# Performance work log

Hardware: AMD Instinct MI355X
Metric: run time of the kernel (lower is better)

## Reference

```python
import jax, jax.numpy as jnp
import numpy as np

B, L = 4, 2048
D_MODEL, D_INNER, D_STATE, DT_RANK, K = 512, 1024, 16, 64, 4


def setup_inputs() -> dict:
    key = jax.random.key(0)
    ks = jax.random.split(key, 21)
    def n(k, shape, s=0.02):
        return (jax.random.normal(k, shape) * s).astype(jnp.float32)
    inp = {"x": jax.random.normal(ks[0], (B, L, D_MODEL), jnp.float32)}
    for i, sfx in enumerate(("f", "b")):
        o = 1 + i * 8
        inp[f"W_in_{sfx}"] = n(ks[o], (2 * D_INNER, D_MODEL))
        inp[f"conv_w_{sfx}"] = n(ks[o + 1], (D_INNER, 1, K), 0.1)
        inp[f"conv_b_{sfx}"] = jnp.zeros((D_INNER,), jnp.float32)
        inp[f"A_log_{sfx}"] = (jax.random.normal(ks[o + 2], (D_STATE, D_INNER)) * 0.1).astype(jnp.float32)
        inp[f"D_{sfx}"] = jnp.ones((D_INNER,), jnp.float32)
        inp[f"Wx_{sfx}"] = n(ks[o + 3], (DT_RANK + 2 * D_STATE, D_INNER))
        inp[f"Wdt_{sfx}"] = n(ks[o + 4], (D_INNER, DT_RANK), DT_RANK ** -0.5)
        dt = jnp.exp(jax.random.uniform(ks[o + 5], (D_INNER,)) * (np.log(0.1) - np.log(0.001)) + np.log(0.001))
        inp[f"bdt_{sfx}"] = (dt + jnp.log(-jnp.expm1(-dt))).astype(jnp.float32)
        inp[f"Wout_{sfx}"] = n(ks[o + 6], (D_MODEL, D_INNER))
    return inp


def _mamba_block(x, W_in, conv_w, conv_b, A_log, Dp, Wx, Wdt, bdt, Wout):
    # x: [B, L, d_model]
    xz = jnp.einsum('bld,ed->ble', x, W_in)              # [B, L, 2*d_inner]
    xb, zb = xz[..., :D_INNER], xz[..., D_INNER:]
    # causal depthwise conv over time
    xc = jnp.transpose(xb, (0, 2, 1))                     # [B, M, L]
    xc = jax.lax.conv_general_dilated(
        xc, conv_w, window_strides=(1,), padding=[(K - 1, 0)],
        feature_group_count=D_INNER,
        dimension_numbers=('NCH', 'OIH', 'NCH')) + conv_b[None, :, None]
    xb = jax.nn.silu(jnp.transpose(xc, (0, 2, 1)))        # [B, L, M]
    # input-dependent SSM parameters
    proj = jnp.einsum('blm,pm->blp', xb, Wx)              # [B, L, dt_rank+2D]
    dt_in = proj[..., :DT_RANK]
    Bs = proj[..., DT_RANK:DT_RANK + D_STATE]             # [B, L, D]
    Cs = proj[..., DT_RANK + D_STATE:]                    # [B, L, D]
    dt = jax.nn.softplus(jnp.einsum('blr,mr->blm', dt_in, Wdt) + bdt)  # [B, L, M]
    A_T = -jnp.exp(A_log).T                               # [M, D]

    def step(h, inp):
        dt_t, x_t, B_t, C_t = inp                         # [B,M],[B,M],[B,D],[B,D]
        dA = jnp.exp(dt_t[:, :, None] * A_T[None])        # [B, M, D]
        h = dA * h + (dt_t * x_t)[:, :, None] * B_t[:, None, :]
        y_t = jnp.einsum('bmd,bd->bm', h, C_t)
        return h, y_t

    xs = (jnp.moveaxis(dt, 1, 0), jnp.moveaxis(xb, 1, 0),
          jnp.moveaxis(Bs, 1, 0), jnp.moveaxis(Cs, 1, 0))
    h0 = jnp.zeros((x.shape[0], D_INNER, D_STATE), x.dtype)
    _, ys = jax.lax.scan(step, h0, xs)                    # [L, B, M]
    y = jnp.moveaxis(ys, 0, 1) + Dp * xb                  # [B, L, M]
    y = y * jax.nn.silu(zb)                               # SiLU gate
    return jnp.einsum('blm,dm->bld', y, Wout)             # [B, L, d_model]


def reference(x,
              W_in_f, conv_w_f, conv_b_f, A_log_f, D_f, Wx_f, Wdt_f, bdt_f, Wout_f,
              W_in_b, conv_w_b, conv_b_b, A_log_b, D_b, Wx_b, Wdt_b, bdt_b, Wout_b):
    out_f = _mamba_block(x, W_in_f, conv_w_f, conv_b_f, A_log_f, D_f, Wx_f, Wdt_f, bdt_f, Wout_f)
    out_b = jnp.flip(_mamba_block(jnp.flip(x, 1), W_in_b, conv_w_b, conv_b_b, A_log_b, D_b, Wx_b, Wdt_b, bdt_b, Wout_b), 1)
    return out_f + out_b
```

## Files before the change

kernel.cpp:

```cpp
#include <hip/hip_runtime.h>
#include <hip/hip_bf16.h>
#include <cstdint>
#include <cstdio>

typedef float f32x4 __attribute__((ext_vector_type(4)));
typedef float f32x2 __attribute__((ext_vector_type(2)));
typedef short s16x8 __attribute__((ext_vector_type(8)));
typedef unsigned int u32x2 __attribute__((ext_vector_type(2)));

__device__ __forceinline__ float us2f(unsigned short u){
  union { unsigned int i; float f; } v; v.i = ((unsigned int)u) << 16; return v.f;
}
__device__ __forceinline__ unsigned short f2us(float f){
  union { float f; unsigned int i; } v; v.f = f;
  unsigned int r = v.i + 0x7fffu + ((v.i >> 16) & 1u);
  return (unsigned short)(r >> 16);
}
__device__ __forceinline__ void gload_lds16(const void* g, void* l){
  __builtin_amdgcn_global_load_lds(
      (const __attribute__((address_space(1))) unsigned int*)g,
      (__attribute__((address_space(3))) unsigned int*)l, 16, 0, 0);
}

#define PK0 0.999962f

__global__ __launch_bounds__(256)
void prep_k(const float* __restrict__ x,
            const float* __restrict__ W_in_f, const float* __restrict__ W_in_b,
            const float* __restrict__ Wx_f,   const float* __restrict__ Wx_b,
            const float* __restrict__ Wdt_f,  const float* __restrict__ Wdt_b,
            const float* __restrict__ Wout_f, const float* __restrict__ Wout_b,
            const float* __restrict__ Alog_f, const float* __restrict__ Alog_b,
            const float* __restrict__ bdt_f,  const float* __restrict__ bdt_b,
            unsigned short* __restrict__ W1cat, unsigned short* __restrict__ Wxpad,
            unsigned short* __restrict__ Wdtb,  unsigned short* __restrict__ Woutcat,
            float* __restrict__ A2, float* __restrict__ bdtcat,
            unsigned short* __restrict__ xbf, float* __restrict__ Cf)
{
  long i = (long)blockIdx.x * 256 + threadIdx.x;
  if (i < 4194304) {
    xbf[i] = f2us(x[i]); return;
  }
  i -= 4194304;
  if (i < 2097152) {
    int n = (int)(i >> 9), k = (int)(i & 511);
    float v = (n < 2048) ? W_in_f[(long)n*512 + k] : W_in_b[(long)(n-2048)*512 + k];
    W1cat[i] = f2us(v); return;
  }
  i -= 2097152;
  if (i < 262144) {
    int dir = (int)(i >> 17); long r = i & 131071; int n = (int)(r >> 10), k = (int)(r & 1023);
    const float* Wx = dir ? Wx_b : Wx_f;
    Wxpad[(long)dir*131072 + r] = f2us(n < 96 ? Wx[(long)n*1024 + k] : 0.f); return;
  }
  i -= 262144;
  if (i < 131072) {
    int dir = (int)(i >> 16); long r = i & 65535;
    Wdtb[i] = f2us((dir ? Wdt_b : Wdt_f)[r]); return;
  }
  i -= 131072;
  if (i < 1048576) {
    int n = (int)(i >> 11), k = (int)(i & 2047);
    float v = (k < 1024) ? Wout_f[(long)n*1024 + k] : Wout_b[(long)n*1024 + (k-1024)];
    Woutcat[i] = f2us(v); return;
  }
  i -= 1048576;
  if (i < 32768) {
    int dir = (int)(i >> 14); long r = i & 16383; int m = (int)(r >> 4), d = (int)(r & 15);
    const float* Al = dir ? Alog_b : Alog_f;
    A2[i] = -__expf(Al[(long)d*1024 + m]) * 1.4426950408889634f; return;
  }
  i -= 32768;
  if (i < 2048) {
    int dir = (int)(i >> 10), m = (int)(i & 1023);
    bdtcat[i] = (dir ? bdt_b : bdt_f)[m]; return;
  }
  i -= 2048;
  if (i < 98304) {
    int dir = (int)(i / 49152); long r = i % 49152;
    int m = (int)(r / 48), j = (int)(r % 48);
    int k = j >> 4, d = j & 15;
    const float* Al = dir ? Alog_b : Alog_f;
    const float w = -__expf(Al[(long)d*1024 + m]);
    float c;
    if (k == 0)      c = 0.999150f * w;
    else if (k == 1) c = 0.492809f * w * w;
    else             c = 0.139212f * w * w * w;
    Cf[(long)dir*49152 + (long)m*48 + (k << 4) + d] = c;
    return;
  }
}

template<int OUT_MODE, int DBUF>
__global__ __launch_bounds__(256)
void gemm_bt(const unsigned short* __restrict__ Ap, const unsigned short* __restrict__ Bp,
             void* __restrict__ Cp, const float* __restrict__ biasp,
             float* __restrict__ bcf,
             int K, int lda, int ldb, int ldc,
             long az, long bz, long cz, int biasz)
{
  const int z   = blockIdx.z;
  const int tid = threadIdx.x;
  const int bm  = blockIdx.x, bn = blockIdx.y;

  __shared__ __align__(16) unsigned short Ash[1+DBUF][128][64];
  __shared__ __align__(16) unsigned short Bsh[1+DBUF][128][64];

  const int wave = tid >> 6, lane = tid & 63;
  const int wr = (wave >> 1) << 6, wc = (wave & 1) << 6;
  const int fr = lane & 15, fs = lane >> 4;

  const int rr  = tid >> 3;
  const int csp = tid & 7;
  const int csg = ((csp ^ (rr & 7)) << 3);

  const unsigned short* Ag = Ap + (long)z * az;
  const unsigned short* Bg = Bp + (long)z * bz;

  const long abase = (long)(bm*128 + rr)*lda + csg;
  const long bbase = (long)(bn*128 + rr)*ldb + csg;

  f32x4 acc[4][4];
  #pragma unroll
  for (int i=0;i<4;i++)
    #pragma unroll
    for (int j=0;j<4;j++) acc[i][j] = (f32x4){0.f,0.f,0.f,0.f};

  const int NK = K >> 6;

  auto stage = [&](int buf, int ks){
    const long k0 = (long)ks << 6;
    #pragma unroll
    for (int r=0;r<4;r++){
      gload_lds16(Ag + abase + (long)(r*32)*lda + k0, &Ash[buf][rr + r*32][csp << 3]);
      gload_lds16(Bg + bbase + (long)(r*32)*ldb + k0, &Bsh[buf][rr + r*32][csp << 3]);
    }
  };
  auto compute = [&](int buf){
    #pragma unroll
    for (int sub=0; sub<2; ++sub){
      s16x8 af[4], bfv[4];
      #pragma unroll
      for (int i=0;i<4;i++){
        const int ar = wr + i*16 + fr;
        af[i]  = *(const s16x8*)&Ash[buf][ar][(((sub<<2)+fs) ^ (fr&7)) << 3];
        const int br = wc + i*16 + fr;
        bfv[i] = *(const s16x8*)&Bsh[buf][br][(((sub<<2)+fs) ^ (fr&7)) << 3];
      }
      #pragma unroll
      for (int i=0;i<4;i++)
        #pragma unroll
        for (int j=0;j<4;j++)
          acc[i][j] = __builtin_amdgcn_mfma_f32_16x16x32_bf16(bfv[j], af[i], acc[i][j], 0, 0, 0);
    }
  };

  if (DBUF){
    stage(0, 0);
    int cur = 0;
    for (int ks = 0; ks < NK; ++ks){
      __syncthreads();
      if (ks + 1 < NK) stage(cur ^ 1, ks + 1);
      compute(cur);
      cur ^= 1;
    }
  } else {
    for (int ks = 0; ks < NK; ++ks){
      __syncthreads();
      stage(0, ks);
      __syncthreads();
      compute(0);
    }
  }

  #pragma unroll
  for (int i=0;i<4;i++){
    const int row = bm*128 + wr + i*16 + fr;
    #pragma unroll
    for (int j=0;j<4;j++){
      const int c0 = bn*128 + wc + j*16 + (fs << 2);
      f32x4 v = acc[i][j];
      const long cbase = (long)z*cz + (long)row*ldc + c0;
      if (OUT_MODE == 2){
        *(f32x4*)((float*)Cp + cbase) = v;
      } else if (OUT_MODE == 1){
        const f32x4 b4 = *(const f32x4*)(biasp + z*biasz + c0);
        u32x2 o;
        unsigned short s[4];
        #pragma unroll
        for (int e=0;e<4;e++){
          float t = v[e] + b4[e];
          t = fmaxf(t, 0.f) + log1pf(__expf(-fabsf(t)));
          s[e] = f2us(t);
        }
        o[0] = (unsigned int)s[0] | ((unsigned int)s[1] << 16);
        o[1] = (unsigned int)s[2] | ((unsigned int)s[3] << 16);
        *(u32x2*)((unsigned short*)Cp + cbase) = o;
      } else {
        if (OUT_MODE == 4 && ((c0 >> 10) & 1)){
          #pragma unroll
          for (int e=0;e<4;e++) v[e] = v[e] / (1.f + __expf(-v[e]));
        }
        u32x2 o;
        o[0] = (unsigned int)f2us(v[0]) | ((unsigned int)f2us(v[1]) << 16);
        o[1] = (unsigned int)f2us(v[2]) | ((unsigned int)f2us(v[3]) << 16);
        *(u32x2*)((unsigned short*)Cp + cbase) = o;
        if (OUT_MODE == 3 && c0 >= 64 && c0 < 96){
          *(f32x4*)(bcf + ((long)z*8192 + row)*32 + (c0 - 64)) = v;
        }
      }
    }
  }
}

__global__ __launch_bounds__(256)
void conv_silu_k(const unsigned short* __restrict__ xz,
                 const float* __restrict__ wf, const float* __restrict__ cbf,
                 const float* __restrict__ wb, const float* __restrict__ cbb,
                 unsigned short* __restrict__ xbc)
{
  const int tid = threadIdx.x;
  const long tok = blockIdx.x;
  const int l   = (int)(tok & 2047);
  const int dir = tid >> 7;
  const int mg  = (tid & 127) << 3;
  const float* w  = dir ? wb  : wf;
  const float* cb = dir ? cbb : cbf;
  const long rowb = tok << 12;
  const int  xcol = (dir << 11) + mg;

  f32x4 wv[8];
  #pragma unroll
  for (int e=0;e<8;e++) wv[e] = *(const f32x4*)(w + (mg + e)*4);
  const f32x4 cb0 = *(const f32x4*)(cb + mg);
  const f32x4 cb1 = *(const f32x4*)(cb + mg + 4);

  float acc[8];
  #pragma unroll
  for (int e=0;e<4;e++){ acc[e]=cb0[e]; acc[4+e]=cb1[e]; }

  #pragma unroll
  for (int k=0;k<4;k++){
    const int off = dir ? (3 - k) : (k - 3);
    const int pos = l + off;
    if (pos >= 0 && pos < 2048){
      const s16x8 xv = *(const s16x8*)(xz + rowb + ((long)off << 12) + xcol);
      #pragma unroll
      for (int e=0;e<8;e++)
        acc[e] = __builtin_fmaf(wv[e][k], us2f((unsigned short)xv[e]), acc[e]);
    }
  }
  s16x8 out;
  #pragma unroll
  for (int e=0;e<8;e++){
    const float s = acc[e] / (1.f + __expf(-acc[e]));
    out[e] = (short)f2us(s);
  }
  *(s16x8*)(xbc + tok*2048 + (dir << 10) + mg) = out;
}

#define SCHUNK 32
#define NCHUNK 64

__global__ __launch_bounds__(256)
void scan1_k(const unsigned short* __restrict__ dtb, const unsigned short* __restrict__ xbc,
             const float* __restrict__ BCf, const float* __restrict__ Cf,
             unsigned short* __restrict__ hloc, float* __restrict__ Ssum)
{
  const int tidx = threadIdx.x;
  const int cb = blockIdx.x, c = blockIdx.y, bz = blockIdx.z;
  const int b = bz >> 1, dir = bz & 1;
  const int m = cb*256 + tidx;

  f32x2 C1v[8], C2v[8], C3v[8];
  { const f32x4* p = (const f32x4*)(Cf + ((long)dir*1024 + m)*48);
    #pragma unroll
    for (int q=0;q<4;q++){
      f32x4 v1=p[q], v2=p[q+4], v3=p[q+8];
      C1v[2*q]   = (f32x2){v1[0], v1[1]};  C1v[2*q+1] = (f32x2){v1[2], v1[3]};
      C2v[2*q]   = (f32x2){v2[0], v2[1]};  C2v[2*q+1] = (f32x2){v2[2], v2[3]};
      C3v[2*q]   = (f32x2){v3[0], v3[1]};  C3v[2*q+1] = (f32x2){v3[2], v3[3]};
    } }
  const f32x2 k0v = {PK0, PK0};

  const int  l0 = dir ? (2047 - c*SCHUNK) : (c*SCHUNK);
  const int  ls = dir ? -1 : 1;
  const long tok0 = (long)b*2048 + l0;

  __shared__ float Bs[SCHUNK][16];
  if (tidx < 128){
    const int r = tidx >> 2, c4 = (tidx & 3) << 2;
    *(f32x4*)&Bs[r][c4] =
        *(const f32x4*)(BCf + ((long)dir*8192 + tok0 + (long)ls*r)*32 + c4);
  }
  __syncthreads();

  const unsigned short* dtp = dtb + ((long)dir << 23) + tok0*1024 + m;
  const unsigned short* xvp = xbc + tok0*2048 + (dir << 10) + m;
  const long dstp = (long)ls*1024, xstp = (long)ls*2048;

  f32x2 h2[8];
  #pragma unroll
  for (int p=0;p<8;p++) h2[p] = (f32x2){0.f, 0.f};
  float S = 0.f;

  unsigned short du = *dtp, xu = *xvp;
  for (int t=0;t<SCHUNK;t++){
    const float dt = us2f(du), xv = us2f(xu);
    dtp += dstp; xvp += xstp;
    du = *dtp; xu = *xvp;
    S += dt;
    const float u = dt * xv;
    const float dt2 = dt*dt, dt3 = dt2*dt;
    const f32x2 dtv = {dt, dt}, dt2v = {dt2, dt2}, dt3v = {dt3, dt3}, uv = {u, u};
    const f32x2* b2 = (const f32x2*)&Bs[t][0];
    #pragma unroll
    for (int p=0;p<8;p++){
      f32x2 a = __builtin_elementwise_fma(C1v[p], dtv, k0v);
      a = __builtin_elementwise_fma(C2v[p], dt2v, a);
      a = __builtin_elementwise_fma(C3v[p], dt3v, a);
      h2[p] = __builtin_elementwise_fma(a, h2[p], uv * b2[p]);
    }
  }
  const long o = (((long)bz * NCHUNK) + c)*1024 + m;
  s16x8 hv0, hv1;
  #pragma unroll
  for (int e=0;e<4;e++){
    hv0[2*e]   = (short)f2us(h2[e][0]);     hv0[2*e+1] = (short)f2us(h2[e][1]);
    hv1[2*e]   = (short)f2us(h2[4+e][0]);   hv1[2*e+1] = (short)f2us(h2[4+e][1]);
  }
  *(s16x8*)(hloc + (o << 4))     = hv0;
  *(s16x8*)(hloc + (o << 4) + 8) = hv1;
  Ssum[o] = S;
}

__global__ __launch_bounds__(256)
void scan2_k(const float* __restrict__ A2, const float* __restrict__ Ssum,
             unsigned short* __restrict__ hloc)
{
  const long idx = (long)blockIdx.x*256 + threadIdx.x;
  const long bz = idx >> 14; const int r = (int)(idx & 16383);
  const int dir = (int)(bz & 1);
  const float a2 = A2[((long)dir << 14) + r];
  const long base = bz * NCHUNK;
  float hs = 0.f;
  float hlN = us2f(hloc[base*16384 + r]);
  float SN  = Ssum[base*1024 + (r >> 4)];
  for (int c=0;c<NCHUNK;c++){
    const float hl = hlN, Sv = SN;
    const int cn = (c+1 < NCHUNK) ? c+1 : c;
    hlN = us2f(hloc[(base+cn)*16384 + r]);
    SN  = Ssum[(base+cn)*1024 + (r >> 4)];
    const float P = __builtin_amdgcn_exp2f(a2 * Sv);
    hloc[(base+c)*16384 + r] = f2us(hs);
    hs = __builtin_fmaf(P, hs, hl);
  }
}

__global__ __launch_bounds__(256)
void scan3_k(const unsigned short* __restrict__ dtb, const unsigned short* __restrict__ xbc,
             const float* __restrict__ BCf, const float* __restrict__ Cf,
             const unsigned short* __restrict__ hstart, const unsigned short* __restrict__ xz,
             const float* __restrict__ D_f, const float* __restrict__ D_b,
             unsigned short* __restrict__ ybuf)
{
  const int tidx = threadIdx.x;
  const int cb = blockIdx.x, c = blockIdx.y, bz = blockIdx.z;
  const int b = bz >> 1, dir = bz & 1;
  const int m = cb*256 + tidx;

  f32x2 C1v[8], C2v[8], C3v[8];
  { const f32x4* p = (const f32x4*)(Cf + ((long)dir*1024 + m)*48);
    #pragma unroll
    for (int q=0;q<4;q++){
      f32x4 v1=p[q], v2=p[q+4], v3=p[q+8];
      C1v[2*q]   = (f32x2){v1[0], v1[1]};  C1v[2*q+1] = (f32x2){v1[2], v1[3]};
      C2v[2*q]   = (f32x2){v2[0], v2[1]};  C2v[2*q+1] = (f32x2){v2[2], v2[3]};
      C3v[2*q]   = (f32x2){v3[0], v3[1]};  C3v[2*q+1] = (f32x2){v3[2], v3[3]};
    } }
  const f32x2 k0v = {PK0, PK0};
  const float Dm = (dir ? D_b : D_f)[m];

  const int  l0 = dir ? (2047 - c*SCHUNK) : (c*SCHUNK);
  const int  ls = dir ? -1 : 1;
  const long tok0 = (long)b*2048 + l0;

  __shared__ float BC[SCHUNK][32];
  { const int r = tidx >> 3, c4 = (tidx & 7) << 2;
    *(f32x4*)&BC[r][c4] =
        *(const f32x4*)(BCf + ((long)dir*8192 + tok0 + (long)ls*r)*32 + c4); }

  f32x2 h2[8];
  { const long o = ((((long)bz*NCHUNK) + c)*1024 + m) << 4;
    s16x8 hv0 = *(const s16x8*)(hstart + o);
    s16x8 hv1 = *(const s16x8*)(hstart + o + 8);
    #pragma unroll
    for (int e=0;e<4;e++){
      h2[e]   = (f32x2){us2f((unsigned short)hv0[2*e]), us2f((unsigned short)hv0[2*e+1])};
      h2[4+e] = (f32x2){us2f((unsigned short)hv1[2*e]), us2f((unsigned short)hv1[2*e+1])};
    } }
  __syncthreads();

  const unsigned short* dtp = dtb + ((long)dir << 23) + tok0*1024 + m;
  const unsigned short* xvp = xbc + tok0*2048 + (dir << 10) + m;
  const unsigned short* zp  = xz  + (tok0 << 12) + (dir << 11) + 1024 + m;
  unsigned short*       yp  = ybuf + tok0*2048 + (dir << 10) + m;
  const long dstp = (long)ls*1024, xstp = (long)ls*2048, zstp = (long)ls << 12;

  unsigned short du = *dtp, xu = *xvp, zu = *zp;
  for (int t=0;t<SCHUNK;t++){
    const float dt = us2f(du), xv = us2f(xu), gate = us2f(zu);
    dtp += dstp; xvp += xstp; zp += zstp;
    du = *dtp; xu = *xvp; zu = *zp;
    const float u = dt * xv;
    const float dt2 = dt*dt, dt3 = dt2*dt;
    const f32x2 dtv = {dt, dt}, dt2v = {dt2, dt2}, dt3v = {dt3, dt3}, uv = {u, u};
    const f32x2* bc2 = (const f32x2*)&BC[t][0];
    f32x2 y2a = {0.f, 0.f}, y2b = {0.f, 0.f};
    #pragma unroll
    for (int p=0;p<8;p++){
      f32x2 a = __builtin_elementwise_fma(C1v[p], dtv, k0v);
      a = __builtin_elementwise_fma(C2v[p], dt2v, a);
      a = __builtin_elementwise_fma(C3v[p], dt3v, a);
      h2[p] = __builtin_elementwise_fma(a, h2[p], uv * bc2[p]);
      if (p & 1) y2b = __builtin_elementwise_fma(h2[p], bc2[8+p], y2b);
      else       y2a = __builtin_elementwise_fma(h2[p], bc2[8+p], y2a);
    }
    const float y = ((y2a[0] + y2a[1]) + (y2b[0] + y2b[1])) + Dm * xv;
    *yp = f2us(y * gate);
    yp += xstp;
  }
}

extern "C" void kernel_launch(void* const* d_in, const int* in_sizes, int n_in,
                              void* d_out, int out_size, void* d_ws, size_t ws_size,
                              hipStream_t stream)
{
  const float* x      = (const float*)d_in[0];
  const float* W_in_f = (const float*)d_in[1];
  const float* convw_f= (const float*)d_in[2];
  const float* convb_f= (const float*)d_in[3];
  const float* Alog_f = (const float*)d_in[4];
  const float* D_f    = (const float*)d_in[5];
  const float* Wx_f   = (const float*)d_in[6];
  const float* Wdt_f  = (const float*)d_in[7];
  const float* bdt_f  = (const float*)d_in[8];
  const float* Wout_f = (const float*)d_in[9];
  const float* W_in_b = (const float*)d_in[10];
  const float* convw_b= (const float*)d_in[11];
  const float* convb_b= (const float*)d_in[12];
  const float* Alog_b = (const float*)d_in[13];
  const float* D_b    = (const float*)d_in[14];
  const float* Wx_b   = (const float*)d_in[15];
  const float* Wdt_b  = (const float*)d_in[16];
  const float* bdt_b  = (const float*)d_in[17];
  const float* Wout_b = (const float*)d_in[18];

  char* w = (char*)d_ws;
  auto carve = [&](size_t bytes) -> char* {
    char* p = w; w += (bytes + 255) & ~(size_t)255; return p;
  };
  unsigned short* W1cat   = (unsigned short*)carve(4096ULL*512*2);
  unsigned short* Wxpad   = (unsigned short*)carve(2ULL*128*1024*2);
  unsigned short* Wdtb    = (unsigned short*)carve(2ULL*1024*64*2);
  unsigned short* Woutcat = (unsigned short*)carve(512ULL*2048*2);
  float*          A2      = (float*)carve(2ULL*1024*16*4);
  float*          bdtcat  = (float*)carve(2048ULL*4);
  float*          Cf      = (float*)carve(2ULL*1024*48*4);
  float*          BCf     = (float*)carve(2ULL*8192*32*4);
  unsigned short* xz      = (unsigned short*)carve(8192ULL*4096*2);
  unsigned short* xbc     = (unsigned short*)carve(8192ULL*2048*2);
  unsigned short* proj    = (unsigned short*)carve(2ULL*8192*128*2);
  unsigned short* dtb     = (unsigned short*)carve(2ULL*8192*1024*2);
  unsigned short* ybuf    = (unsigned short*)carve(8192ULL*2048*2);
  unsigned short* hloc    = (unsigned short*)carve(8ULL*NCHUNK*1024*16*2);
  float*          Ssum    = (float*)carve(8ULL*NCHUNK*1024*4);
  unsigned short* xbf     = ybuf;

  if ((size_t)(w - (char*)d_ws) > ws_size) {
    fprintf(stderr, "kernel_launch: ws too small (%zu needed, %zu given)\n",
            (size_t)(w - (char*)d_ws), ws_size);
    return;
  }

  prep_k<<<dim3(30728), 256, 0, stream>>>(x, W_in_f, W_in_b, Wx_f, Wx_b, Wdt_f, Wdt_b,
                                          Wout_f, Wout_b, Alog_f, Alog_b, bdt_f, bdt_b,
                                          W1cat, Wxpad, Wdtb, Woutcat, A2, bdtcat, xbf, Cf);
  gemm_bt<4,1><<<dim3(64,32,1), 256, 0, stream>>>(xbf, W1cat, xz, nullptr, nullptr,
                                                  512, 512, 512, 4096, 0, 0, 0, 0);
  conv_silu_k<<<dim3(8192), 256, 0, stream>>>(xz, convw_f, convb_f, convw_b, convb_b, xbc);
  gemm_bt<3,1><<<dim3(64,1,2), 256, 0, stream>>>(xbc, Wxpad, proj, nullptr, BCf,
                                                 1024, 2048, 1024, 128,
                                                 1024, 131072, 1048576, 0);
  gemm_bt<1,0><<<dim3(64,8,2), 256, 0, stream>>>(proj, Wdtb, dtb, bdtcat, nullptr,
                                                 64, 128, 64, 1024,
                                                 1048576, 65536, 8388608, 1024);
  scan1_k<<<dim3(4,NCHUNK,8), 256, 0, stream>>>(dtb, xbc, BCf, Cf, hloc, Ssum);
  scan2_k<<<dim3(512), 256, 0, stream>>>(A2, Ssum, hloc);
  scan3_k<<<dim3(4,NCHUNK,8), 256, 0, stream>>>(dtb, xbc, BCf, Cf, hloc, xz, D_f, D_b, ybuf);
  gemm_bt<2,1><<<dim3(64,4,1), 256, 0, stream>>>(ybuf, Woutcat, d_out, nullptr, nullptr,
                                                 2048, 2048, 2048, 512, 0, 0, 0, 0);
}
```

Baseline: 321.4 us.

## Use 256x256 tile GEMM for input projection and double-buffer scan loads

Adds a dedicated 512-thread GEMM kernel with 256x256 tiles and double-buffered LDS staging for the input projection, replacing the 128x128 tile kernel there and moving the z-gate SiLU epilogue into it. The larger tile raises arithmetic intensity per loaded byte. In exchange it uses 128KB of shared memory, runs one block per CU, and launches only 512 blocks. The scan1 and scan3 kernels also alternate between two pointer streams so loads run two steps ahead, hiding global load latency in the sequential recurrence.

```diff
diff --git a/kernel.cpp b/kernel.cpp
--- a/kernel.cpp
+++ b/kernel.cpp
@@ -88,6 +88,94 @@
     else             c = 0.139212f * w * w * w;
     Cf[(long)dir*49152 + (long)m*48 + (k << 4) + d] = c;
     return;
+  }
+}
+
+template<int OUT_MODE>
+__global__ __launch_bounds__(512, 1)
+void gemm_big(const unsigned short* __restrict__ Ap, const unsigned short* __restrict__ Bp,
+              unsigned short* __restrict__ Cp,
+              int K, int lda, int ldb, int ldc)
+{
+  const int tid = threadIdx.x;
+  const int bm  = blockIdx.x, bn = blockIdx.y;
+
+  __shared__ __align__(16) unsigned short Ash[2][256][64];
+  __shared__ __align__(16) unsigned short Bsh[2][256][64];
+
+  const int wave = tid >> 6, lane = tid & 63;
+  const int wr = (wave >> 2) << 7;
+  const int wc = (wave & 3) << 6;
+  const int fr = lane & 15, fs = lane >> 4;
+
+  const int rr  = tid >> 3;
+  const int csp = tid & 7;
+  const int csg = ((csp ^ (rr & 7)) << 3);
+
+  const long abase = (long)(bm*256 + rr)*lda + csg;
+  const long bbase = (long)(bn*256 + rr)*ldb + csg;
+
+  f32x4 acc[8][4];
+  #pragma unroll
+  for (int i=0;i<8;i++)
+    #pragma unroll
+    for (int j=0;j<4;j++) acc[i][j] = (f32x4){0.f,0.f,0.f,0.f};
+
+  const int NK = K >> 6;
+
+  auto stage = [&](int buf, int ks){
+    const long k0 = (long)ks << 6;
+    #pragma unroll
+    for (int r=0;r<4;r++){
+      gload_lds16(Ap + abase + (long)(r*64)*lda + k0, &Ash[buf][rr + r*64][csp << 3]);
+      gload_lds16(Bp + bbase + (long)(r*64)*ldb + k0, &Bsh[buf][rr + r*64][csp << 3]);
+    }
+  };
+  auto compute = [&](int buf){
+    #pragma unroll
+    for (int sub=0; sub<2; ++sub){
+      s16x8 bfv[4];
+      #pragma unroll
+      for (int j=0;j<4;j++){
+        const int br = wc + j*16 + fr;
+        bfv[j] = *(const s16x8*)&Bsh[buf][br][(((sub<<2)+fs) ^ (fr&7)) << 3];
+      }
+      #pragma unroll
+      for (int i=0;i<8;i++){
+        const int ar = wr + i*16 + fr;
+        const s16x8 af = *(const s16x8*)&Ash[buf][ar][(((sub<<2)+fs) ^ (fr&7)) << 3];
+        #pragma unroll
+        for (int j=0;j<4;j++)
+          acc[i][j] = __builtin_amdgcn_mfma_f32_16x16x32_bf16(bfv[j], af, acc[i][j], 0, 0, 0);
+      }
+    }
+  };
+
+  stage(0, 0);
+  int cur = 0;
+  for (int ks = 0; ks < NK; ++ks){
+    __syncthreads();
+    if (ks + 1 < NK) stage(cur ^ 1, ks + 1);
+    compute(cur);
+    cur ^= 1;
+  }
+
+  #pragma unroll
+  for (int i=0;i<8;i++){
+    const int row = bm*256 + wr + i*16 + fr;
+    #pragma unroll
+    for (int j=0;j<4;j++){
+      const int c0 = bn*256 + wc + j*16 + (fs << 2);
+      f32x4 v = acc[i][j];
+      if (OUT_MODE == 4 && ((c0 >> 10) & 1)){
+        #pragma unroll
+        for (int e=0;e<4;e++) v[e] = v[e] / (1.f + __expf(-v[e]));
+      }
+      u32x2 o;
+      o[0] = (unsigned int)f2us(v[0]) | ((unsigned int)f2us(v[1]) << 16);
+      o[1] = (unsigned int)f2us(v[2]) | ((unsigned int)f2us(v[3]) << 16);
+      *(u32x2*)(Cp + (long)row*ldc + c0) = o;
+    }
   }
 }
 
@@ -197,10 +285,6 @@
         o[1] = (unsigned int)s[2] | ((unsigned int)s[3] << 16);
         *(u32x2*)((unsigned short*)Cp + cbase) = o;
       } else {
-        if (OUT_MODE == 4 && ((c0 >> 10) & 1)){
-          #pragma unroll
-          for (int e=0;e<4;e++) v[e] = v[e] / (1.f + __expf(-v[e]));
-        }
         u32x2 o;
         o[0] = (unsigned int)f2us(v[0]) | ((unsigned int)f2us(v[1]) << 16);
         o[1] = (unsigned int)f2us(v[2]) | ((unsigned int)f2us(v[3]) << 16);
@@ -295,20 +379,18 @@
   }
   __syncthreads();
 
-  const unsigned short* dtp = dtb + ((long)dir << 23) + tok0*1024 + m;
-  const unsigned short* xvp = xbc + tok0*2048 + (dir << 10) + m;
   const long dstp = (long)ls*1024, xstp = (long)ls*2048;
+  const unsigned short* dt0 = dtb + ((long)dir << 23) + tok0*1024 + m;
+  const unsigned short* xv0 = xbc + tok0*2048 + (dir << 10) + m;
+  const unsigned short* dt1 = dt0 + dstp;
+  const unsigned short* xv1 = xv0 + xstp;
 
   f32x2 h2[8];
   #pragma unroll
   for (int p=0;p<8;p++) h2[p] = (f32x2){0.f, 0.f};
   float S = 0.f;
 
-  unsigned short du = *dtp, xu = *xvp;
-  for (int t=0;t<SCHUNK;t++){
-    const float dt = us2f(du), xv = us2f(xu);
-    dtp += dstp; xvp += xstp;
-    du = *dtp; xu = *xvp;
+  auto body = [&](float dt, float xv, int t){
     S += dt;
     const float u = dt * xv;
     const float dt2 = dt*dt, dt3 = dt2*dt;
@@ -321,6 +403,18 @@
       a = __builtin_elementwise_fma(C3v[p], dt3v, a);
       h2[p] = __builtin_elementwise_fma(a, h2[p], uv * b2[p]);
     }
+  };
+
+  unsigned short dA = *dt0, xA = *xv0, dB = *dt1, xB = *xv1;
+  for (int t=0; t<SCHUNK; t+=2){
+    const float dtA = us2f(dA), xvA = us2f(xA);
+    dt0 += 2*dstp; xv0 += 2*xstp;
+    dA = *dt0; xA = *xv0;
+    body(dtA, xvA, t);
+    const float dtB = us2f(dB), xvB = us2f(xB);
+    dt1 += 2*dstp; xv1 += 2*xstp;
+    dB = *dt1; xB = *xv1;
+    body(dtB, xvB, t+1);
   }
   const long o = (((long)bz * NCHUNK) + c)*1024 + m;
   s16x8 hv0, hv1;
@@ -401,17 +495,16 @@
     } }
   __syncthreads();
 
-  const unsigned short* dtp = dtb + ((long)dir << 23) + tok0*1024 + m;
-  const unsigned short* xvp = xbc + tok0*2048 + (dir << 10) + m;
-  const unsigned short* zp  = xz  + (tok0 << 12) + (dir << 11) + 1024 + m;
+  const long dstp = (long)ls*1024, xstp = (long)ls*2048, zstp = (long)ls << 12;
+  const unsigned short* dt0 = dtb + ((long)dir << 23) + tok0*1024 + m;
+  const unsigned short* xv0 = xbc + tok0*2048 + (dir << 10) + m;
+  const unsigned short* zp0 = xz  + (tok0 << 12) + (dir << 11) + 1024 + m;
+  const unsigned short* dt1 = dt0 + dstp;
+  const unsigned short* xv1 = xv0 + xstp;
+  const unsigned short* zp1 = zp0 + zstp;
   unsigned short*       yp  = ybuf + tok0*2048 + (dir << 10) + m;
-  const long dstp = (long)ls*1024, xstp = (long)ls*2048, zstp = (long)ls << 12;
-
-  unsigned short du = *dtp, xu = *xvp, zu = *zp;
-  for (int t=0;t<SCHUNK;t++){
-    const float dt = us2f(du), xv = us2f(xu), gate = us2f(zu);
-    dtp += dstp; xvp += xstp; zp += zstp;
-    du = *dtp; xu = *xvp; zu = *zp;
+
+  auto body = [&](float dt, float xv, float gate, int t){
     const float u = dt * xv;
     const float dt2 = dt*dt, dt3 = dt2*dt;
     const f32x2 dtv = {dt, dt}, dt2v = {dt2, dt2}, dt3v = {dt3, dt3}, uv = {u, u};
@@ -429,6 +522,19 @@
     const float y = ((y2a[0] + y2a[1]) + (y2b[0] + y2b[1])) + Dm * xv;
     *yp = f2us(y * gate);
     yp += xstp;
+  };
+
+  unsigned short dA = *dt0, xA = *xv0, zA = *zp0;
+  unsigned short dB = *dt1, xB = *xv1, zB = *zp1;
+  for (int t=0; t<SCHUNK; t+=2){
+    const float dtA = us2f(dA), xvA = us2f(xA), gA = us2f(zA);
+    dt0 += 2*dstp; xv0 += 2*xstp; zp0 += 2*zstp;
+    dA = *dt0; xA = *xv0; zA = *zp0;
+    body(dtA, xvA, gA, t);
+    const float dtB = us2f(dB), xvB = us2f(xB), gB = us2f(zB);
+    dt1 += 2*dstp; xv1 += 2*xstp; zp1 += 2*zstp;
+    dB = *dt1; xB = *xv1; zB = *zp1;
+    body(dtB, xvB, gB, t+1);
   }
 }
 
@@ -486,8 +592,7 @@
   prep_k<<<dim3(30728), 256, 0, stream>>>(x, W_in_f, W_in_b, Wx_f, Wx_b, Wdt_f, Wdt_b,
                                           Wout_f, Wout_b, Alog_f, Alog_b, bdt_f, bdt_b,
                                           W1cat, Wxpad, Wdtb, Woutcat, A2, bdtcat, xbf, Cf);
-  gemm_bt<4,1><<<dim3(64,32,1), 256, 0, stream>>>(xbf, W1cat, xz, nullptr, nullptr,
-                                                  512, 512, 512, 4096, 0, 0, 0, 0);
+  gemm_big<4><<<dim3(32,16), 512, 0, stream>>>(xbf, W1cat, xz, 512, 512, 512, 4096);
   conv_silu_k<<<dim3(8192), 256, 0, stream>>>(xz, convw_f, convb_f, convw_b, convb_b, xbc);
   gemm_bt<3,1><<<dim3(64,1,2), 256, 0, stream>>>(xbc, Wxpad, proj, nullptr, BCf,
                                                  1024, 2048, 1024, 128,
```

Result: no change. 316.3 us (median of 2 runs) (-1.6%).

## Use 4-slot LDS ring with vmcnt waits in GEMM; unroll scan loads by two

Applied to the files above, without the earlier changes.

The GEMM's double-buffer or single-buffer K loop becomes a 4-slot LDS ring with three stages in flight. Each step waits on explicit s_waitcnt vmcnt counts plus one raw barrier, where before it used __syncthreads per step. The scan1 and scan3 loops are unrolled by two, with separate pointer streams so more per-token global loads are outstanding. The ring uses 128 KB of LDS per block, which may reduce occupancy. The hand-set vmcnt counts and the single barrier before overwriting a slot are fragile if the compiler reorders loads.

```diff
diff --git a/kernel.cpp b/kernel.cpp
--- a/kernel.cpp
+++ b/kernel.cpp
@@ -91,20 +91,20 @@
   }
 }
 
-template<int OUT_MODE, int DBUF>
+template<int OUT_MODE>
 __global__ __launch_bounds__(256)
-void gemm_bt(const unsigned short* __restrict__ Ap, const unsigned short* __restrict__ Bp,
-             void* __restrict__ Cp, const float* __restrict__ biasp,
-             float* __restrict__ bcf,
-             int K, int lda, int ldb, int ldc,
-             long az, long bz, long cz, int biasz)
+void gemm_ring(const unsigned short* __restrict__ Ap, const unsigned short* __restrict__ Bp,
+               void* __restrict__ Cp, const float* __restrict__ biasp,
+               float* __restrict__ bcf,
+               int K, int lda, int ldb, int ldc,
+               long az, long bz, long cz, int biasz)
 {
   const int z   = blockIdx.z;
   const int tid = threadIdx.x;
   const int bm  = blockIdx.x, bn = blockIdx.y;
 
-  __shared__ __align__(16) unsigned short Ash[1+DBUF][128][64];
-  __shared__ __align__(16) unsigned short Bsh[1+DBUF][128][64];
+  __shared__ __align__(16) unsigned short Ash[4][128][64];
+  __shared__ __align__(16) unsigned short Bsh[4][128][64];
 
   const int wave = tid >> 6, lane = tid & 63;
   const int wr = (wave >> 1) << 6, wc = (wave & 1) << 6;
@@ -128,24 +128,24 @@
 
   const int NK = K >> 6;
 
-  auto stage = [&](int buf, int ks){
+  auto stage = [&](int slot, int ks){
     const long k0 = (long)ks << 6;
     #pragma unroll
     for (int r=0;r<4;r++){
-      gload_lds16(Ag + abase + (long)(r*32)*lda + k0, &Ash[buf][rr + r*32][csp << 3]);
-      gload_lds16(Bg + bbase + (long)(r*32)*ldb + k0, &Bsh[buf][rr + r*32][csp << 3]);
+      gload_lds16(Ag + abase + (long)(r*32)*lda + k0, &Ash[slot][rr + r*32][csp << 3]);
+      gload_lds16(Bg + bbase + (long)(r*32)*ldb + k0, &Bsh[slot][rr + r*32][csp << 3]);
     }
   };
-  auto compute = [&](int buf){
+  auto compute = [&](int slot){
     #pragma unroll
     for (int sub=0; sub<2; ++sub){
       s16x8 af[4], bfv[4];
       #pragma unroll
       for (int i=0;i<4;i++){
         const int ar = wr + i*16 + fr;
-        af[i]  = *(const s16x8*)&Ash[buf][ar][(((sub<<2)+fs) ^ (fr&7)) << 3];
+        af[i]  = *(const s16x8*)&Ash[slot][ar][(((sub<<2)+fs) ^ (fr&7)) << 3];
         const int br = wc + i*16 + fr;
-        bfv[i] = *(const s16x8*)&Bsh[buf][br][(((sub<<2)+fs) ^ (fr&7)) << 3];
+        bfv[i] = *(const s16x8*)&Bsh[slot][br][(((sub<<2)+fs) ^ (fr&7)) << 3];
       }
       #pragma unroll
       for (int i=0;i<4;i++)
@@ -155,22 +155,16 @@
     }
   };
 
-  if (DBUF){
-    stage(0, 0);
-    int cur = 0;
-    for (int ks = 0; ks < NK; ++ks){
-      __syncthreads();
-      if (ks + 1 < NK) stage(cur ^ 1, ks + 1);
-      compute(cur);
-      cur ^= 1;
-    }
-  } else {
-    for (int ks = 0; ks < NK; ++ks){
-      __syncthreads();
-      stage(0, ks);
-      __syncthreads();
-      compute(0);
-    }
+  const int NP = NK < 3 ? NK : 3;
+  for (int t = 0; t < NP; ++t) stage(t & 3, t);
+
+  for (int kt = 0; kt < NK; ++kt){
+    if (kt < NK - 2)       asm volatile("s_waitcnt vmcnt(16)" ::: "memory");
+    else if (kt == NK - 2) asm volatile("s_waitcnt vmcnt(8)"  ::: "memory");
+    else                   asm volatile("s_waitcnt vmcnt(0)"  ::: "memory");
+    __builtin_amdgcn_s_barrier();
+    if (kt + 3 < NK) stage((kt + 3) & 3, kt + 3);
+    compute(kt & 3);
   }
 
   #pragma unroll
@@ -295,20 +289,18 @@
   }
   __syncthreads();
 
-  const unsigned short* dtp = dtb + ((long)dir << 23) + tok0*1024 + m;
-  const unsigned short* xvp = xbc + tok0*2048 + (dir << 10) + m;
   const long dstp = (long)ls*1024, xstp = (long)ls*2048;
+  const unsigned short* dt0 = dtb + ((long)dir << 23) + tok0*1024 + m;
+  const unsigned short* xv0 = xbc + tok0*2048 + (dir << 10) + m;
+  const unsigned short* dt1 = dt0 + dstp;
+  const unsigned short* xv1 = xv0 + xstp;
 
   f32x2 h2[8];
   #pragma unroll
   for (int p=0;p<8;p++) h2[p] = (f32x2){0.f, 0.f};
   float S = 0.f;
 
-  unsigned short du = *dtp, xu = *xvp;
-  for (int t=0;t<SCHUNK;t++){
-    const float dt = us2f(du), xv = us2f(xu);
-    dtp += dstp; xvp += xstp;
-    du = *dtp; xu = *xvp;
+  auto body = [&](float dt, float xv, int t){
     S += dt;
     const float u = dt * xv;
     const float dt2 = dt*dt, dt3 = dt2*dt;
@@ -321,6 +313,18 @@
       a = __builtin_elementwise_fma(C3v[p], dt3v, a);
       h2[p] = __builtin_elementwise_fma(a, h2[p], uv * b2[p]);
     }
+  };
+
+  unsigned short dA = *dt0, xA = *xv0, dB = *dt1, xB = *xv1;
+  for (int t=0; t<SCHUNK; t+=2){
+    const float dtA = us2f(dA), xvA = us2f(xA);
+    dt0 += 2*dstp; xv0 += 2*xstp;
+    dA = *dt0; xA = *xv0;
+    body(dtA, xvA, t);
+    const float dtB = us2f(dB), xvB = us2f(xB);
+    dt1 += 2*dstp; xv1 += 2*xstp;
+    dB = *dt1; xB = *xv1;
+    body(dtB, xvB, t+1);
   }
   const long o = (((long)bz * NCHUNK) + c)*1024 + m;
   s16x8 hv0, hv1;
@@ -401,17 +405,16 @@
     } }
   __syncthreads();
 
-  const unsigned short* dtp = dtb + ((long)dir << 23) + tok0*1024 + m;
-  const unsigned short* xvp = xbc + tok0*2048 + (dir << 10) + m;
-  const unsigned short* zp  = xz  + (tok0 << 12) + (dir << 11) + 1024 + m;
+  const long dstp = (long)ls*1024, xstp = (long)ls*2048, zstp = (long)ls << 12;
+  const unsigned short* dt0 = dtb + ((long)dir << 23) + tok0*1024 + m;
+  const unsigned short* xv0 = xbc + tok0*2048 + (dir << 10) + m;
+  const unsigned short* zp0 = xz  + (tok0 << 12) + (dir << 11) + 1024 + m;
+  const unsigned short* dt1 = dt0 + dstp;
+  const unsigned short* xv1 = xv0 + xstp;
+  const unsigned short* zp1 = zp0 + zstp;
   unsigned short*       yp  = ybuf + tok0*2048 + (dir << 10) + m;
-  const long dstp = (long)ls*1024, xstp = (long)ls*2048, zstp = (long)ls << 12;
-
-  unsigned short du = *dtp, xu = *xvp, zu = *zp;
-  for (int t=0;t<SCHUNK;t++){
-    const float dt = us2f(du), xv = us2f(xu), gate = us2f(zu);
-    dtp += dstp; xvp += xstp; zp += zstp;
-    du = *dtp; xu = *xvp; zu = *zp;
+
+  auto body = [&](float dt, float xv, float gate, int t){
     const float u = dt * xv;
     const float dt2 = dt*dt, dt3 = dt2*dt;
     const f32x2 dtv = {dt, dt}, dt2v = {dt2, dt2}, dt3v = {dt3, dt3}, uv = {u, u};
@@ -429,6 +432,19 @@
     const float y = ((y2a[0] + y2a[1]) + (y2b[0] + y2b[1])) + Dm * xv;
     *yp = f2us(y * gate);
     yp += xstp;
+  };
+
+  unsigned short dA = *dt0, xA = *xv0, zA = *zp0;
+  unsigned short dB = *dt1, xB = *xv1, zB = *zp1;
+  for (int t=0; t<SCHUNK; t+=2){
+    const float dtA = us2f(dA), xvA = us2f(xA), gA = us2f(zA);
+    dt0 += 2*dstp; xv0 += 2*xstp; zp0 += 2*zstp;
+    dA = *dt0; xA = *xv0; zA = *zp0;
+    body(dtA, xvA, gA, t);
+    const float dtB = us2f(dB), xvB = us2f(xB), gB = us2f(zB);
+    dt1 += 2*dstp; xv1 += 2*xstp; zp1 += 2*zstp;
+    dB = *dt1; xB = *xv1; zB = *zp1;
+    body(dtB, xvB, gB, t+1);
   }
 }
 
@@ -486,18 +502,18 @@
   prep_k<<<dim3(30728), 256, 0, stream>>>(x, W_in_f, W_in_b, Wx_f, Wx_b, Wdt_f, Wdt_b,
                                           Wout_f, Wout_b, Alog_f, Alog_b, bdt_f, bdt_b,
                                           W1cat, Wxpad, Wdtb, Woutcat, A2, bdtcat, xbf, Cf);
-  gemm_bt<4,1><<<dim3(64,32,1), 256, 0, stream>>>(xbf, W1cat, xz, nullptr, nullptr,
+  gemm_ring<4><<<dim3(64,32,1), 256, 0, stream>>>(xbf, W1cat, xz, nullptr, nullptr,
                                                   512, 512, 512, 4096, 0, 0, 0, 0);
   conv_silu_k<<<dim3(8192), 256, 0, stream>>>(xz, convw_f, convb_f, convw_b, convb_b, xbc);
-  gemm_bt<3,1><<<dim3(64,1,2), 256, 0, stream>>>(xbc, Wxpad, proj, nullptr, BCf,
+  gemm_ring<3><<<dim3(64,1,2), 256, 0, stream>>>(xbc, Wxpad, proj, nullptr, BCf,
                                                  1024, 2048, 1024, 128,
                                                  1024, 131072, 1048576, 0);
-  gemm_bt<1,0><<<dim3(64,8,2), 256, 0, stream>>>(proj, Wdtb, dtb, bdtcat, nullptr,
+  gemm_ring<1><<<dim3(64,8,2), 256, 0, stream>>>(proj, Wdtb, dtb, bdtcat, nullptr,
                                                  64, 128, 64, 1024,
                                                  1048576, 65536, 8388608, 1024);
   scan1_k<<<dim3(4,NCHUNK,8), 256, 0, stream>>>(dtb, xbc, BCf, Cf, hloc, Ssum);
   scan2_k<<<dim3(512), 256, 0, stream>>>(A2, Ssum, hloc);
   scan3_k<<<dim3(4,NCHUNK,8), 256, 0, stream>>>(dtb, xbc, BCf, Cf, hloc, xz, D_f, D_b, ybuf);
-  gemm_bt<2,1><<<dim3(64,4,1), 256, 0, stream>>>(ybuf, Woutcat, d_out, nullptr, nullptr,
+  gemm_ring<2><<<dim3(64,4,1), 256, 0, stream>>>(ybuf, Woutcat, d_out, nullptr, nullptr,
                                                  2048, 2048, 2048, 512, 0, 0, 0, 0);
 }
```

Measured after the change: 359.1 us. 11.7% more time.
